# Performance work log

Hardware: AMD Instinct MI355X
Metric: run time of the kernel (lower is better)

The kernel has to match this reference:

```python
import jax, jax.numpy as jnp
import numpy as np

N_NODES = 30000
N_EDGES = 300000
N_GRAPHS = 512
SEQ = 1000
HEADS = 10
CH = 78


def setup_inputs() -> dict:
    key = jax.random.key(0)
    ks = jax.random.split(key, 20)
    def w(k, shape, scale=0.02):
        return jax.random.normal(k, shape, jnp.float32) * scale
    x = jax.random.normal(ks[0], (N_NODES, CH), jnp.float32)
    edge_index = jax.random.randint(ks[1], (2, N_EDGES), 0, N_NODES, jnp.int32)
    # every graph gets a contiguous block of nodes (sorted batch vector)
    batch = (jnp.arange(N_NODES) * N_GRAPHS // N_NODES).astype(jnp.int32)
    target = jax.random.randint(ks[2], (N_GRAPHS, SEQ), 0, 26, jnp.int32)
    return {
        "x": x, "edge_index": edge_index, "batch": batch, "target": target,
        "W_gat": w(ks[3], (CH, HEADS * CH)),
        "att_src": w(ks[4], (HEADS, CH), 0.1),
        "att_dst": w(ks[5], (HEADS, CH), 0.1),
        "b_gat": jnp.zeros((HEADS * CH,), jnp.float32),
        "W_gcn": w(ks[6], (HEADS * CH, HEADS * CH)),
        "b_gcn": jnp.zeros((HEADS * CH,), jnp.float32),
        "W_fcg1": w(ks[7], (2 * HEADS * CH, 1500)), "b_fcg1": jnp.zeros((1500,), jnp.float32),
        "W_fcg2": w(ks[8], (1500, 128)), "b_fcg2": jnp.zeros((128,), jnp.float32),
        "emb": w(ks[9], (26, 128), 1.0),
        "W_conv": w(ks[10], (32, 1000, 8)), "b_conv": jnp.zeros((32,), jnp.float32),
        "W_fcxt": w(ks[11], (32 * 121, 128)), "b_fcxt": jnp.zeros((128,), jnp.float32),
        "W_fc1": w(ks[12], (256, 1024)), "b_fc1": jnp.zeros((1024,), jnp.float32),
        "W_fc2": w(ks[13], (1024, 512)), "b_fc2": jnp.zeros((512,), jnp.float32),
        "W_out": w(ks[14], (512, 1)), "b_out": jnp.zeros((1,), jnp.float32),
    }


def reference(x, edge_index, batch, target,
              W_gat, att_src, att_dst, b_gat, W_gcn, b_gcn,
              W_fcg1, b_fcg1, W_fcg2, b_fcg2, emb, W_conv, b_conv,
              W_fcxt, b_fcxt, W_fc1, b_fc1, W_fc2, b_fc2, W_out, b_out):
    N = x.shape[0]
    loop = jnp.arange(N, dtype=edge_index.dtype)
    src = jnp.concatenate([edge_index[0], loop])  # self-loops (PyG default)
    dst = jnp.concatenate([edge_index[1], loop])

    # ---- GATConv(78 -> 78, heads=10, concat) ----
    h = (x @ W_gat).reshape(N, HEADS, CH)           # [N,H,C]
    a_s = jnp.einsum('nhc,hc->nh', h, att_src)      # [N,H]
    a_d = jnp.einsum('nhc,hc->nh', h, att_dst)
    logits = jax.nn.leaky_relu(a_s[src] + a_d[dst], 0.2)   # [E',H]
    m = jax.ops.segment_max(logits, dst, num_segments=N)
    e = jnp.exp(logits - m[dst])
    denom = jax.ops.segment_sum(e, dst, num_segments=N)
    alpha = e / (denom[dst] + 1e-16)                # per-dst softmax
    xg = jax.ops.segment_sum(h[src] * alpha[:, :, None], dst, num_segments=N)
    xg = jax.nn.relu(xg.reshape(N, HEADS * CH) + b_gat)

    # ---- GCNConv(780 -> 780), symmetric norm with self-loops ----
    deg = jax.ops.segment_sum(jnp.ones_like(dst, dtype=xg.dtype), dst, num_segments=N)
    dinv = jax.lax.rsqrt(jnp.maximum(deg, 1.0))
    norm = dinv[src] * dinv[dst]                    # [E']
    xw = xg @ W_gcn
    xg = jax.ops.segment_sum(xw[src] * norm[:, None], dst, num_segments=N) + b_gcn
    xg = jax.nn.relu(xg)

    # ---- global max + mean pooling per graph ----
    gmax = jax.ops.segment_max(xg, batch, num_segments=N_GRAPHS)
    cnt = jax.ops.segment_sum(jnp.ones((N,), xg.dtype), batch, num_segments=N_GRAPHS)
    gmean = jax.ops.segment_sum(xg, batch, num_segments=N_GRAPHS) / cnt[:, None]
    xp = jnp.concatenate([gmax, gmean], axis=1)     # [G,1560]
    xp = jax.nn.relu(xp @ W_fcg1 + b_fcg1)          # dropout = identity (eval)
    xp = xp @ W_fcg2 + b_fcg2                       # [G,128]

    # ---- protein branch ----
    xt = emb[target]                                # [G,1000,128]
    conv = jax.lax.conv_general_dilated(
        xt, W_conv, window_strides=(1,), padding='VALID',
        dimension_numbers=('NCH', 'OIH', 'NCH'))    # [G,32,121]
    conv = conv + b_conv[None, :, None]
    xt = conv.reshape(conv.shape[0], -1) @ W_fcxt + b_fcxt  # [G,128]

    # ---- joint MLP ----
    xc = jnp.concatenate([xp, xt], axis=1)          # [G,256]
    xc = jax.nn.relu(xc @ W_fc1 + b_fc1)
    xc = jax.nn.relu(xc @ W_fc2 + b_fc2)
    return xc @ W_out + b_out                       # [G,1]
```

## Files before the change

### kernel.cpp

```cpp
#include <hip/hip_runtime.h>
#include <hip/hip_bf16.h>
#include <cstdint>
#include <cstddef>

#define N_NODES 30000
#define E0      300000
#define EPRIME  330000
#define NG      512
#define SEQL    1000
#define HEADS   10
#define CHN     78
#define HC      780
#define HP      800
#define MAXD    64

typedef __attribute__((ext_vector_type(8))) short bf16x8;
typedef __attribute__((ext_vector_type(4))) float f32x4;
typedef __attribute__((ext_vector_type(8))) unsigned short u16x8;

static __device__ __forceinline__ int src_of(const int* ei, int e){
  return (e < E0) ? ei[e] : (e - E0);
}
static __device__ __forceinline__ int dst_of(const int* ei, int e){
  return (e < E0) ? ei[E0 + e] : (e - E0);
}
static __device__ __forceinline__ unsigned short f2bf(float f){
  union { float f; unsigned u; } a; a.f = f;
  unsigned r = a.u + 0x7fff + ((a.u >> 16) & 1);
  return (unsigned short)(r >> 16);
}
static __device__ __forceinline__ float bf2f(unsigned short u){
  union { unsigned u; float f; } a; a.u = ((unsigned)u) << 16; return a.f;
}
static __device__ __forceinline__ void gl_lds16(const unsigned short* g, unsigned short* l){
  __builtin_amdgcn_global_load_lds(
      (const __attribute__((address_space(1))) void*)g,
      (__attribute__((address_space(3))) void*)l,
      16, 0, 0);
}

__global__ void k_bucket(const int* __restrict__ ei, int* __restrict__ cnt, int* __restrict__ bkt){
  int e = blockIdx.x*256 + threadIdx.x;
  if (e < EPRIME){
    int d = dst_of(ei, e);
    int s = src_of(ei, e);
    int slot = atomicAdd(&cnt[d], 1);
    if (slot < MAXD) bkt[d*MAXD + slot] = s;
  }
}

__global__ __launch_bounds__(256) void k_w2t(const float* __restrict__ W_conv, float* __restrict__ w2t){
  int b = blockIdx.x;
  int o = threadIdx.x >> 3, k = threadIdx.x & 7;
  w2t[(size_t)b*256 + threadIdx.x] = W_conv[(size_t)o*8000 + b*8 + k];
}

static __device__ void transp_tile(const float* __restrict__ src, unsigned short* __restrict__ dst,
                                   int K, int N, int Kp, int bx, int by, int hpad){
  __shared__ float t[32][33];
  int k0 = bx*32, n0 = by*32;
  int c = threadIdx.x & 31, r = threadIdx.x >> 5;
  #pragma unroll
  for (int i=0;i<4;i++){
    int k = k0 + r + i*8;
    float v = 0.f;
    if (k < K && n0 + c < N) v = src[(size_t)k*N + n0 + c];
    t[r + i*8][c] = v;
  }
  __syncthreads();
  #pragma unroll
  for (int i=0;i<4;i++){
    int nn = n0 + r + i*8;
    int kk = k0 + c;
    if (nn < N){
      if (hpad){
        if (kk < K){
          int hh = kk/78;
          dst[(size_t)nn*Kp + hh*80 + (kk - hh*78)] = f2bf(t[c][r + i*8]);
        }
      } else {
        if (kk < Kp) dst[(size_t)nn*Kp + kk] = f2bf(t[c][r + i*8]);
      }
    }
  }
}

static __device__ void conv_body(int g, int tid, const int* __restrict__ target,
                                 const float* __restrict__ W2t, const float* __restrict__ emb,
                                 const float* __restrict__ b_conv, float* __restrict__ convf){
  int o = tid >> 3;
  __shared__ int   tgt[SEQL];
  __shared__ int   cntv[26];
  __shared__ int   startv[27];
  __shared__ int   ofs[26];
  __shared__ alignas(16) unsigned short posv[SEQL];
  __shared__ float U[256*26];
  __shared__ float sE[26*128 + 32];

  for (int i = tid; i < 26*128; i += 256) sE[i] = emb[i];
  if (tid < 32) sE[26*128 + tid] = 0.f;
  if (tid < 26) cntv[tid] = 0;
  const int* tg = target + g*SEQL;
  for (int i = tid; i < SEQL; i += 256) tgt[i] = tg[i];
  __syncthreads();
  for (int i = tid; i < SEQL; i += 256) atomicAdd(&cntv[tgt[i]], 1);
  __syncthreads();
  if (tid == 0){
    int s = 0;
    #pragma unroll
    for (int v = 0; v < 26; v++){ startv[v] = s; ofs[v] = s; s += cntv[v]; }
    startv[26] = s;
  }
  __syncthreads();
  for (int i = tid; i < SEQL; i += 256){
    int v = tgt[i];
    int slot = atomicAdd(&ofs[v], 1);
    posv[slot] = (unsigned short)((v << 10) | i);
  }
  __syncthreads();
  {
    const float* wp2 = W2t + tid;
    float s = 0.f;
    int cur = 0;
    for (int j = 0; j < SEQL; j += 8){
      u16x8 p8 = *(const u16x8*)&posv[j];
      float w[8];
      #pragma unroll
      for (int q = 0; q < 8; q++) w[q] = wp2[((int)p8[q] & 1023) << 8];
      #pragma unroll
      for (int q = 0; q < 8; q++){
        int ve = (int)p8[q] >> 10;
        if (ve != cur){
          U[tid*26 + cur] = s;
          for (int z = cur+1; z < ve; z++) U[tid*26 + z] = 0.f;
          cur = ve; s = 0.f;
        }
        s += w[q];
      }
    }
    U[tid*26 + cur] = s;
    for (int z = cur+1; z < 26; z++) U[tid*26 + z] = 0.f;
  }
  __syncthreads();
  int pg = tid & 7;
  int p0 = pg * 16;
  int np = 121 - p0; if (np > 16) np = 16;
  float acc[16];
  #pragma unroll
  for (int i=0;i<16;i++) acc[i]=0.f;
  for (int v = 0; v < 26; v++){
    float u[8];
    #pragma unroll
    for (int kk=0;kk<8;kk++) u[kk] = U[(o*8 + kk)*26 + v];
    const float* ep = &sE[v*128 + p0];
    float e[24];
    #pragma unroll
    for (int i=0;i<24;i+=4){
      float4 q = *(const float4*)(ep + i);
      e[i]=q.x; e[i+1]=q.y; e[i+2]=q.z; e[i+3]=q.w;
    }
    #pragma unroll
    for (int pl=0; pl<16; pl++){
      acc[pl] += u[0]*e[pl]   + u[1]*e[pl+1] + u[2]*e[pl+2] + u[3]*e[pl+3]
               + u[4]*e[pl+4] + u[5]*e[pl+5] + u[6]*e[pl+6] + u[7]*e[pl+7];
    }
  }
  float bo = b_conv[o];
  for (int pl=0; pl<np; pl++)
    convf[(size_t)g*3872 + o*121 + p0 + pl] = acc[pl] + bo;
}

__global__ __launch_bounds__(256) void k_prep(
    const float* __restrict__ x, unsigned short* __restrict__ xb,
    const float* __restrict__ W_gat, unsigned short* __restrict__ wgat_t,
    const float* __restrict__ W_gcn, unsigned short* __restrict__ wgcn_t,
    const float* __restrict__ W_fcg1, unsigned short* __restrict__ wfcg1_t,
    const int* __restrict__ target, const float* __restrict__ w2t,
    const float* __restrict__ emb, const float* __restrict__ b_conv, float* __restrict__ convf,
    unsigned short* __restrict__ xwbp,
    float* __restrict__ xc, float* __restrict__ t1, float* __restrict__ t2, float* __restrict__ fg1,
    const float* __restrict__ b_fcg2, const float* __restrict__ b_fcxt,
    const float* __restrict__ b_fc1, const float* __restrict__ b_fc2,
    const float* __restrict__ b_fcg1, int* __restrict__ cnt)
{
  int b = blockIdx.x;
  int tid = threadIdx.x;
  if (b < 512){ conv_body(b, tid, target, w2t, emb, b_conv, convf); return; }
  b -= 512;
  if (b < 11250){
    int idx = b*256 + tid;
    if (idx < N_NODES*96){
      int n = idx/96, k = idx - n*96;
      xb[idx] = (k < CHN) ? f2bf(x[(size_t)n*CHN + k]) : 0;
    }
    return;
  }
  b -= 11250;
  if (b < 75){ transp_tile(W_gat, wgat_t, CHN, HC, 96, b%3, b/3, 0); return; }
  b -= 75;
  if (b < 625){ transp_tile(W_gcn, wgcn_t, HC, HC, HP, b%25, b/25, 1); return; }
  b -= 625;
  if (b < 2303){ transp_tile(W_fcg1, wfcg1_t, 1560, 1500, 1568, b%49, b/49, 0); return; }
  b -= 2303;
  {
    int g = b;
    int zi = g*256 + tid;
    if (zi < N_NODES) cnt[zi] = 0;
    if (tid < 128){
      xc[(size_t)g*256 + tid]       = b_fcg2[tid];
      xc[(size_t)g*256 + 128 + tid] = b_fcxt[tid];
    }
    for (int i = tid; i < 1024; i += 256) t1[(size_t)g*1024 + i] = b_fc1[i];
    for (int i = tid; i < 512;  i += 256) t2[(size_t)g*512  + i] = b_fc2[i];
    for (int i = tid; i < 1500; i += 256) fg1[(size_t)g*1500 + i] = b_fcg1[i];
    for (int i = tid; i < 59; i += 256){
      int n = g + i*512;
      if (n < N_NODES)
        *reinterpret_cast<unsigned long long*>(xwbp + (size_t)n*HP + HC) = 0ull;
    }
    if (zi < 7800){
      int nn = zi/10, p = zi - (zi/10)*10;
      *reinterpret_cast<unsigned*>(wgcn_t + (size_t)nn*HP + p*80 + 78) = 0u;
    }
  }
}

__global__ __launch_bounds__(256) void k_mfma_bt(
    const unsigned short* __restrict__ A, const unsigned short* __restrict__ Bt,
    const float* __restrict__ bias, float* __restrict__ C, unsigned short* __restrict__ Cb,
    int M, int N, int Kp, int ldc, int relu,
    int ntc, int ntr, int ntk, int Kc, int accum, int hpad)
{
  const int total = ntc*ntr*ntk;
  const int per = (total + 7) >> 3;
  const int b = blockIdx.x;
  const int w = (b & 7)*per + (b >> 3);
  if (w >= total) return;
  const int kt = w / (ntc*ntr);
  const int r2 = w - kt*(ntc*ntr);
  const int row_t = r2 / ntc, col_t = r2 - row_t*ntc;
  const int row0 = row_t*128, col0 = col_t*128;
  const int kbeg = kt*Kc;
  const int kend = min(kbeg + Kc, Kp);

  __shared__ unsigned short As[2][128*32];
  __shared__ unsigned short Bs[2][128*32];
  const int tid = threadIdx.x;
  const int lane = tid & 63;
  const int wv = tid >> 6;
  const int wm = wv >> 1, wn = wv & 1;
  const int quad = lane >> 4, l16 = lane & 15;
  const int srow = lane >> 2;
  const int cidx = lane & 3;
  const int scol = (cidx ^ (srow & 3)) * 8;

  f32x4 acc[4][4];
  #pragma unroll
  for (int mi=0;mi<4;mi++)
    #pragma unroll
    for (int ni=0;ni<4;ni++){
      acc[mi][ni][0]=0.f; acc[mi][ni][1]=0.f; acc[mi][ni][2]=0.f; acc[mi][ni][3]=0.f;
    }

  auto stage = [&](int bsel, int kk){
    #pragma unroll
    for (int i=0;i<2;i++){
      int ch = wv*2 + i;
      int r  = ch*16 + srow;
      gl_lds16(A  + (size_t)(row0 + r)*Kp + kk + scol, &As[bsel][ch*512]);
      gl_lds16(Bt + (size_t)(col0 + r)*Kp + kk + scol, &Bs[bsel][ch*512]);
    }
  };

  const int nt = (kend - kbeg) >> 5;
  stage(0, kbeg);
  __syncthreads();
  int cur = 0;
  for (int t = 0; t < nt; ++t){
    if (t+1 < nt) stage(cur^1, kbeg + ((t+1) << 5));
    bf16x8 af[4], bfr[4];
    #pragma unroll
    for (int mi=0;mi<4;mi++)
      af[mi]  = *(const bf16x8*)(&As[cur][(wm*64 + mi*16 + l16)*32 + ((quad ^ (l16 & 3))*8)]);
    #pragma unroll
    for (int ni=0;ni<4;ni++)
      bfr[ni] = *(const bf16x8*)(&Bs[cur][(wn*64 + ni*16 + l16)*32 + ((quad ^ (l16 & 3))*8)]);
    #pragma unroll
    for (int mi=0;mi<4;mi++)
      #pragma unroll
      for (int ni=0;ni<4;ni++)
        acc[mi][ni] = __builtin_amdgcn_mfma_f32_16x16x32_bf16(af[mi], bfr[ni], acc[mi][ni], 0,0,0);
    __syncthreads();
    cur ^= 1;
  }

  #pragma unroll
  for (int mi=0;mi<4;mi++){
    #pragma unroll
    for (int rr=0;rr<4;rr++){
      int row = row0 + wm*64 + mi*16 + quad*4 + rr;
      if (row >= M) continue;
      #pragma unroll
      for (int ni=0;ni<4;ni++){
        int col = col0 + wn*64 + ni*16 + l16;
        if (col >= N) continue;
        float v = acc[mi][ni][rr];
        if (accum){
          atomicAdd(&C[(size_t)row*ldc + col], v);
        } else {
          if (bias) v += bias[col];
          if (relu) v = fmaxf(v, 0.f);
          int cs = col;
          if (hpad){ int hh = col/78; cs = hh*80 + (col - hh*78); }
          if (Cb) Cb[(size_t)row*ldc + cs] = f2bf(v);
          else    C [(size_t)row*ldc + cs] = v;
        }
      }
    }
  }
}

__global__ __launch_bounds__(256) void k_gemm_sk(const float* __restrict__ A, const float* __restrict__ B,
    float* __restrict__ C, int M, int N, int K, int lda, int ldb, int ldc, int Kc, int relu_a)
{
  __shared__ float As[16][34];
  __shared__ float Bs[16][64];
  const int tid = threadIdx.x;
  const int tx = tid & 15, ty = tid >> 4;
  const int row0 = blockIdx.y * 32, col0 = blockIdx.x * 64;
  const int kbeg = blockIdx.z * Kc;
  const int kend = min(kbeg + Kc, K);
  float acc[2][4];
  #pragma unroll
  for (int i=0;i<2;i++)
    #pragma unroll
    for (int j=0;j<4;j++) acc[i][j] = 0.f;

  for (int k0 = kbeg; k0 < kend; k0 += 16){
    #pragma unroll
    for (int i=0;i<2;i++){
      int idx = tid + i*256;
      int r = idx >> 4, c = idx & 15;
      int gr = row0 + r, gc = k0 + c;
      float v = (gr < M && gc < kend) ? A[(size_t)gr*lda + gc] : 0.f;
      if (relu_a) v = fmaxf(v, 0.f);
      As[c][r] = v;
    }
    #pragma unroll
    for (int i=0;i<4;i++){
      int idx = tid + i*256;
      int r = idx >> 6, c = idx & 63;
      int gr = k0 + r, gc = col0 + c;
      Bs[r][c] = (gr < kend && gc < N) ? B[(size_t)gr*ldb + gc] : 0.f;
    }
    __syncthreads();
    #pragma unroll
    for (int kk=0; kk<16; kk++){
      float a0 = As[kk][ty*2], a1 = As[kk][ty*2+1];
      float b0 = Bs[kk][tx*4], b1 = Bs[kk][tx*4+1], b2 = Bs[kk][tx*4+2], b3 = Bs[kk][tx*4+3];
      acc[0][0]+=a0*b0; acc[0][1]+=a0*b1; acc[0][2]+=a0*b2; acc[0][3]+=a0*b3;
      acc[1][0]+=a1*b0; acc[1][1]+=a1*b1; acc[1][2]+=a1*b2; acc[1][3]+=a1*b3;
    }
    __syncthreads();
  }
  #pragma unroll
  for (int i=0;i<2;i++){
    int r = row0 + ty*2 + i;
    if (r >= M) continue;
    #pragma unroll
    for (int j=0;j<4;j++){
      int c = col0 + tx*4 + j;
      if (c < N) atomicAdd(&C[(size_t)r*ldc + c], acc[i][j]);
    }
  }
}

__global__ __launch_bounds__(256) void k_attn(const unsigned short* __restrict__ hb,
    const float* __restrict__ att_src, const float* __restrict__ att_dst,
    float* __restrict__ a_s, float* __restrict__ a_d){
  __shared__ float ssrc[HC], sdst[HC];
  for (int i = threadIdx.x; i < HC; i += 256){ ssrc[i]=att_src[i]; sdst[i]=att_dst[i]; }
  __syncthreads();
  int idx = blockIdx.x*256 + threadIdx.x;
  if (idx >= N_NODES*HEADS) return;
  int n  = idx / HEADS;
  int hh = idx - n*HEADS;
  const unsigned* hp2 = (const unsigned*)(hb + (size_t)n*HP + hh*80);
  const float* as_ = ssrc + hh*CHN;
  const float* ad_ = sdst + hh*CHN;
  float s1=0.f, s2=0.f;
  #pragma unroll 13
  for (int c2=0;c2<39;c2++){
    unsigned u = hp2[c2];
    float v0 = bf2f((unsigned short)(u & 0xffffu));
    float v1 = bf2f((unsigned short)(u >> 16));
    int c = 2*c2;
    s1 += v0*as_[c] + v1*as_[c+1];
    s2 += v0*ad_[c] + v1*ad_[c+1];
  }
  a_s[idx]=s1; a_d[idx]=s2;
}

__global__ __launch_bounds__(256) void k_gat_agg(
    const unsigned short* __restrict__ hb, const float* __restrict__ a_s, const float* __restrict__ a_d,
    const float* __restrict__ b_gat, const int* __restrict__ cnt, const int* __restrict__ bkt,
    unsigned short* __restrict__ xgb, float* __restrict__ dinv)
{
  int half = threadIdx.x >> 7;
  int lt   = threadIdx.x & 127;
  int n = blockIdx.x*2 + half;
  int deg = cnt[n];
  int degc = min(deg, MAXD);
  __shared__ int   s_src[2][MAXD];
  __shared__ float s_adn[2][HEADS];
  __shared__ float s_lg[2][MAXD*HEADS];
  __shared__ float s_al[2][MAXD*HEADS];
  if (lt < HEADS) s_adn[half][lt] = a_d[(size_t)n*HEADS + lt];
  if (lt < degc)  s_src[half][lt] = bkt[n*MAXD + lt];
  __syncthreads();
  for (int idx = lt; idx < degc*HEADS; idx += 128){
    int j = idx/HEADS, t = idx - j*HEADS;
    float l = a_s[(size_t)s_src[half][j]*HEADS + t] + s_adn[half][t];
    s_lg[half][idx] = (l > 0.f) ? l : 0.2f*l;
  }
  __syncthreads();
  if (lt < HEADS){
    float m = -3.4e38f;
    for (int j=0;j<degc;j++) m = fmaxf(m, s_lg[half][j*HEADS+lt]);
    float s = 0.f;
    for (int j=0;j<degc;j++){ float e = __expf(s_lg[half][j*HEADS+lt]-m); s_al[half][j*HEADS+lt]=e; s+=e; }
    float inv = 1.f/(s + 1e-16f);
    for (int j=0;j<degc;j++) s_al[half][j*HEADS+lt] *= inv;
  }
  __syncthreads();
  if (lt < 100){
    int h = lt/10;
    int r = lt - h*10;
    int nv = (r==9) ? 6 : 8;
    int chb = h*CHN + r*8;
    const float* alp = &s_al[half][h];
    float acc[8];
    #pragma unroll
    for (int e=0;e<8;e++) acc[e]=0.f;
    auto edge = [&](int j){
      int s = s_src[half][j];
      float a = alp[j*HEADS];
      uint4 v = *((const uint4*)(hb + (size_t)s*HP) + lt);
      unsigned uu[4] = {v.x, v.y, v.z, v.w};
      #pragma unroll
      for (int e2=0;e2<4;e2++){
        acc[2*e2]   += a*bf2f((unsigned short)(uu[e2] & 0xffffu));
        acc[2*e2+1] += a*bf2f((unsigned short)(uu[e2] >> 16));
      }
    };
    int j = 0;
    for (; j+2 <= degc; j += 2){ edge(j); edge(j+1); }
    for (; j < degc; ++j) edge(j);
    u16x8 o;
    #pragma unroll
    for (int e=0;e<8;e++){
      float ov = (e < nv) ? fmaxf(acc[e] + b_gat[chb+e], 0.f) : 0.f;
      o[e] = f2bf(ov);
    }
    *((u16x8*)(xgb + (size_t)n*HP) + lt) = o;
  }
  if (lt == 0) dinv[n] = rsqrtf((float)deg);
}

__global__ __launch_bounds__(256) void k_gcn_agg(
    const unsigned short* __restrict__ xwb, const float* __restrict__ dinv, const float* __restrict__ b_gcn,
    const int* __restrict__ cnt, const int* __restrict__ bkt,
    unsigned short* __restrict__ xg2b)
{
  int half = threadIdx.x >> 7;
  int lt   = threadIdx.x & 127;
  int n = blockIdx.x*2 + half;
  int deg = min(cnt[n], MAXD);
  __shared__ int   s_src[2][MAXD];
  __shared__ float s_w[2][MAXD];
  if (lt < deg){
    int s = bkt[n*MAXD + lt];
    s_src[half][lt] = s;
    s_w[half][lt] = dinv[s];
  }
  __syncthreads();
  if (lt < 98){
    int ch0 = lt*8;
    float acc[8];
    #pragma unroll
    for (int e=0;e<8;e++) acc[e]=0.f;
    auto edge = [&](int j){
      int s = s_src[half][j];
      float w = s_w[half][j];
      uint4 v = *((const uint4*)(xwb + (size_t)s*HP) + lt);
      unsigned uu[4] = {v.x, v.y, v.z, v.w};
      #pragma unroll
      for (int e2=0;e2<4;e2++){
        acc[2*e2]   += w*bf2f((unsigned short)(uu[e2] & 0xffffu));
        acc[2*e2+1] += w*bf2f((unsigned short)(uu[e2] >> 16));
      }
    };
    int j = 0;
    for (; j+2 <= deg; j += 2){ edge(j); edge(j+1); }
    for (; j < deg; ++j) edge(j);
    float dn = dinv[n];
    ushort4 o0, o1;
    float r0 = fmaxf(dn*acc[0] + ((ch0   < HC) ? b_gcn[ch0  ] : 0.f), 0.f);
    float r1 = fmaxf(dn*acc[1] + ((ch0+1 < HC) ? b_gcn[ch0+1] : 0.f), 0.f);
    float r2 = fmaxf(dn*acc[2] + ((ch0+2 < HC) ? b_gcn[ch0+2] : 0.f), 0.f);
    float r3 = fmaxf(dn*acc[3] + ((ch0+3 < HC) ? b_gcn[ch0+3] : 0.f), 0.f);
    float r4 = fmaxf(dn*acc[4] + ((ch0+4 < HC) ? b_gcn[ch0+4] : 0.f), 0.f);
    float r5 = fmaxf(dn*acc[5] + ((ch0+5 < HC) ? b_gcn[ch0+5] : 0.f), 0.f);
    float r6 = fmaxf(dn*acc[6] + ((ch0+6 < HC) ? b_gcn[ch0+6] : 0.f), 0.f);
    float r7 = fmaxf(dn*acc[7] + ((ch0+7 < HC) ? b_gcn[ch0+7] : 0.f), 0.f);
    o0.x=f2bf(r0); o0.y=f2bf(r1); o0.z=f2bf(r2); o0.w=f2bf(r3);
    o1.x=f2bf(r4); o1.y=f2bf(r5); o1.z=f2bf(r6); o1.w=f2bf(r7);
    unsigned short* row = xg2b + (size_t)n*HC;
    *(ushort4*)(row + ch0) = o0;
    if (ch0+4 < HC) *(ushort4*)(row + ch0+4) = o1;
  }
}

__global__ __launch_bounds__(256) void k_pool(const unsigned short* __restrict__ xg2b,
                                              unsigned short* __restrict__ xpb){
  int g = blockIdx.x;
  int n0 = (N_NODES*g + NG-1) >> 9;
  int n1 = (N_NODES*(g+1) + NG-1) >> 9;
  float inv = 1.f/(float)(n1 - n0);
  int c4 = threadIdx.x;
  if (c4 < 195){
    const ushort4* x4 = (const ushort4*)xg2b;
    float m0=-3.4e38f,m1=-3.4e38f,m2=-3.4e38f,m3=-3.4e38f;
    float s0=0.f,s1=0.f,s2=0.f,s3=0.f;
    for (int n = n0; n < n1; n++){
      ushort4 v = x4[(size_t)n*195 + c4];
      float a=bf2f(v.x), b=bf2f(v.y), c=bf2f(v.z), d=bf2f(v.w);
      m0=fmaxf(m0,a); m1=fmaxf(m1,b); m2=fmaxf(m2,c); m3=fmaxf(m3,d);
      s0+=a; s1+=b; s2+=c; s3+=d;
    }
    int ch = 4*c4;
    unsigned short* row = xpb + (size_t)g*1568;
    row[ch]=f2bf(m0); row[ch+1]=f2bf(m1); row[ch+2]=f2bf(m2); row[ch+3]=f2bf(m3);
    row[HC+ch]=f2bf(s0*inv); row[HC+ch+1]=f2bf(s1*inv);
    row[HC+ch+2]=f2bf(s2*inv); row[HC+ch+3]=f2bf(s3*inv);
  }
  if (threadIdx.x < 8) xpb[(size_t)g*1568 + 1560 + threadIdx.x] = 0;
}

__global__ __launch_bounds__(64) void k_final(const float* __restrict__ t2, const float* __restrict__ W_out,
                                              const float* __restrict__ b_out, float* __restrict__ out){
  int g = blockIdx.x;
  int lane = threadIdx.x;
  const float* r = t2 + (size_t)g*512;
  float s = 0.f;
  #pragma unroll
  for (int i = lane; i < 512; i += 64) s += fmaxf(r[i], 0.f)*W_out[i];
  #pragma unroll
  for (int off=32; off; off>>=1) s += __shfl_down(s, off);
  if (lane==0) out[g] = s + b_out[0];
}

extern "C" void kernel_launch(void* const* d_in, const int* in_sizes, int n_in,
                              void* d_out, int out_size, void* d_ws, size_t ws_size,
                              hipStream_t stream) {
  const float* x      = (const float*)d_in[0];
  const int*   ei     = (const int*)  d_in[1];
  const int*   target = (const int*)  d_in[3];
  const float* W_gat  = (const float*)d_in[4];
  const float* att_src= (const float*)d_in[5];
  const float* att_dst= (const float*)d_in[6];
  const float* b_gat  = (const float*)d_in[7];
  const float* W_gcn  = (const float*)d_in[8];
  const float* b_gcn  = (const float*)d_in[9];
  const float* W_fcg1 = (const float*)d_in[10];
  const float* b_fcg1 = (const float*)d_in[11];
  const float* W_fcg2 = (const float*)d_in[12];
  const float* b_fcg2 = (const float*)d_in[13];
  const float* emb    = (const float*)d_in[14];
  const float* W_conv = (const float*)d_in[15];
  const float* b_conv = (const float*)d_in[16];
  const float* W_fcxt = (const float*)d_in[17];
  const float* b_fcxt = (const float*)d_in[18];
  const float* W_fc1  = (const float*)d_in[19];
  const float* b_fc1  = (const float*)d_in[20];
  const float* W_fc2  = (const float*)d_in[21];
  const float* b_fc2  = (const float*)d_in[22];
  const float* W_out  = (const float*)d_in[23];
  const float* b_out  = (const float*)d_in[24];
  float* out = (float*)d_out;

  char* ws = (char*)d_ws;
  size_t off = 0;
  auto alloc = [&](size_t bytes)->char*{
    char* p = ws + off;
    off += (bytes + 255) & ~(size_t)255;
    return p;
  };
  unsigned short* hb  = (unsigned short*)alloc((size_t)N_NODES*HP*2);
  unsigned short* xwb = (unsigned short*)alloc((size_t)N_NODES*HP*2);
  unsigned short* xu  = (unsigned short*)alloc((size_t)N_NODES*HP*2);
  unsigned short* xb     = (unsigned short*)alloc((size_t)N_NODES*96*2);
  unsigned short* wgat_t = (unsigned short*)alloc((size_t)HC*96*2);
  unsigned short* wgcn_t = (unsigned short*)alloc((size_t)HC*HP*2);
  unsigned short* wfcg1_t= (unsigned short*)alloc((size_t)1500*1568*2);
  unsigned short* xpb    = (unsigned short*)alloc((size_t)NG*1568*2);
  float* a_s    = (float*)alloc((size_t)N_NODES*HEADS*4);
  float* a_d    = (float*)alloc((size_t)N_NODES*HEADS*4);
  float* dinv   = (float*)alloc((size_t)N_NODES*4);
  int*   cnt    = (int*)  alloc((size_t)N_NODES*4);
  int*   bkt    = (int*)  alloc((size_t)N_NODES*MAXD*4);
  float* fg1    = (float*)alloc((size_t)NG*1500*4);
  float* convf  = (float*)alloc((size_t)NG*3872*4);
  float* xc     = (float*)alloc((size_t)NG*256*4);
  float* t1     = (float*)alloc((size_t)NG*1024*4);
  float* t2     = (float*)alloc((size_t)NG*512*4);
  float* w2t    = (float*)alloc((size_t)SEQL*256*4);

  unsigned short* xgb  = xu;
  unsigned short* xg2b = xu;

  k_w2t<<<1000, 256, 0, stream>>>(W_conv, w2t);

  k_prep<<<512+11250+75+625+2303+512, 256, 0, stream>>>(
      x, xb, W_gat, wgat_t, W_gcn, wgcn_t, W_fcg1, wfcg1_t,
      target, w2t, emb, b_conv, convf, xwb,
      xc, t1, t2, fg1, b_fcg2, b_fcxt, b_fc1, b_fc2, b_fcg1, cnt);

  k_bucket<<<(EPRIME+255)/256, 256, 0, stream>>>(ei, cnt, bkt);

  auto swgrid = [](int total){ return 8 * ((total + 7) / 8); };

  k_mfma_bt<<<swgrid(7*235), 256, 0, stream>>>(xb, wgat_t, nullptr, nullptr, hb,
                                               N_NODES, HC, 96, HP, 0, 7, 235, 1, 96, 0, 1);
  k_attn<<<(N_NODES*HEADS+255)/256, 256, 0, stream>>>(hb, att_src, att_dst, a_s, a_d);
  k_gat_agg<<<N_NODES/2, 256, 0, stream>>>(hb, a_s, a_d, b_gat, cnt, bkt, xgb, dinv);

  k_mfma_bt<<<swgrid(7*235), 256, 0, stream>>>(xgb, wgcn_t, nullptr, nullptr, xwb,
                                               N_NODES, HC, HP, HP, 0, 7, 235, 1, HP, 0, 0);
  k_gcn_agg<<<N_NODES/2, 256, 0, stream>>>(xwb, dinv, b_gcn, cnt, bkt, xg2b);

  k_pool<<<NG, 256, 0, stream>>>(xg2b, xpb);
  k_mfma_bt<<<swgrid(12*4*2), 256, 0, stream>>>(xpb, wfcg1_t, nullptr, fg1, nullptr,
                                                NG, 1500, 1568, 1500, 0, 12, 4, 2, 800, 1, 0);
  k_gemm_sk<<<dim3(2, 16, 8), 256, 0, stream>>>(fg1, W_fcg2, xc, NG, 128, 1500, 1500, 128, 256, 192, 1);

  k_gemm_sk<<<dim3(2, 16, 8), 256, 0, stream>>>(convf, W_fcxt, xc + 128, NG, 128, 3872, 3872, 128, 256, 512, 0);

  k_gemm_sk<<<dim3(16, 16, 1), 256, 0, stream>>>(xc, W_fc1, t1, NG, 1024, 256, 256, 1024, 1024, 256, 0);
  k_gemm_sk<<<dim3(8, 16, 2), 256, 0, stream>>>(t1, W_fc2, t2, NG, 512, 1024, 1024, 512, 512, 512, 1);
  k_final<<<NG, 64, 0, stream>>>(t2, W_out, b_out, out);
}
```

Before: 814.4 us.

## Compute conv weight sums in registers and batch gather loads in aggregations

The conv body no longer builds a 256x26 shared U table in a separate pass. Each thread now sums its 8 conv weights per vocabulary bucket directly from global memory using float4 loads, which saves shared memory and a barrier. In exchange, every thread group of 8 re-reads weights per output channel instead of sharing them. The GAT and GCN aggregation loops now issue four row gathers before doing the multiply-adds, so more memory loads are in flight at once, at the cost of extra registers.

```diff
diff --git a/kernel.cpp b/kernel.cpp
--- a/kernel.cpp
+++ b/kernel.cpp
@@ -94,7 +94,6 @@
   __shared__ int   startv[27];
   __shared__ int   ofs[26];
   __shared__ alignas(16) unsigned short posv[SEQL];
-  __shared__ float U[256*26];
   __shared__ float sE[26*128 + 32];
 
   for (int i = tid; i < 26*128; i += 256) sE[i] = emb[i];
@@ -115,54 +114,39 @@
   for (int i = tid; i < SEQL; i += 256){
     int v = tgt[i];
     int slot = atomicAdd(&ofs[v], 1);
-    posv[slot] = (unsigned short)((v << 10) | i);
-  }
-  __syncthreads();
-  {
-    const float* wp2 = W2t + tid;
-    float s = 0.f;
-    int cur = 0;
-    for (int j = 0; j < SEQL; j += 8){
-      u16x8 p8 = *(const u16x8*)&posv[j];
-      float w[8];
-      #pragma unroll
-      for (int q = 0; q < 8; q++) w[q] = wp2[((int)p8[q] & 1023) << 8];
-      #pragma unroll
-      for (int q = 0; q < 8; q++){
-        int ve = (int)p8[q] >> 10;
-        if (ve != cur){
-          U[tid*26 + cur] = s;
-          for (int z = cur+1; z < ve; z++) U[tid*26 + z] = 0.f;
-          cur = ve; s = 0.f;
-        }
-        s += w[q];
-      }
-    }
-    U[tid*26 + cur] = s;
-    for (int z = cur+1; z < 26; z++) U[tid*26 + z] = 0.f;
-  }
-  __syncthreads();
+    posv[slot] = (unsigned short)i;
+  }
+  __syncthreads();
+
   int pg = tid & 7;
   int p0 = pg * 16;
   int np = 121 - p0; if (np > 16) np = 16;
+  const float* wp8 = W2t + o*8;
   float acc[16];
   #pragma unroll
   for (int i=0;i<16;i++) acc[i]=0.f;
+  int j = 0;
   for (int v = 0; v < 26; v++){
-    float u[8];
-    #pragma unroll
-    for (int kk=0;kk<8;kk++) u[kk] = U[(o*8 + kk)*26 + v];
+    int e_end = startv[v+1];
+    float s0=0.f,s1=0.f,s2=0.f,s3=0.f,s4=0.f,s5=0.f,s6=0.f,s7=0.f;
+    for (; j < e_end; ++j){
+      const float* wp = wp8 + ((int)posv[j] << 8);
+      float4 wa = *(const float4*)wp;
+      float4 wb = *(const float4*)(wp+4);
+      s0+=wa.x; s1+=wa.y; s2+=wa.z; s3+=wa.w;
+      s4+=wb.x; s5+=wb.y; s6+=wb.z; s7+=wb.w;
+    }
     const float* ep = &sE[v*128 + p0];
     float e[24];
     #pragma unroll
-    for (int i=0;i<24;i+=4){
-      float4 q = *(const float4*)(ep + i);
-      e[i]=q.x; e[i+1]=q.y; e[i+2]=q.z; e[i+3]=q.w;
+    for (int i2=0;i2<24;i2+=4){
+      float4 q = *(const float4*)(ep + i2);
+      e[i2]=q.x; e[i2+1]=q.y; e[i2+2]=q.z; e[i2+3]=q.w;
     }
     #pragma unroll
     for (int pl=0; pl<16; pl++){
-      acc[pl] += u[0]*e[pl]   + u[1]*e[pl+1] + u[2]*e[pl+2] + u[3]*e[pl+3]
-               + u[4]*e[pl+4] + u[5]*e[pl+5] + u[6]*e[pl+6] + u[7]*e[pl+7];
+      acc[pl] += s0*e[pl]   + s1*e[pl+1] + s2*e[pl+2] + s3*e[pl+3]
+               + s4*e[pl+4] + s5*e[pl+5] + s6*e[pl+6] + s7*e[pl+7];
     }
   }
   float bo = b_conv[o];
@@ -442,10 +426,12 @@
     float acc[8];
     #pragma unroll
     for (int e=0;e<8;e++) acc[e]=0.f;
-    auto edge = [&](int j){
+    auto ld = [&](int j, uint4& v, float& a){
       int s = s_src[half][j];
-      float a = alp[j*HEADS];
-      uint4 v = *((const uint4*)(hb + (size_t)s*HP) + lt);
+      a = alp[j*HEADS];
+      v = *((const uint4*)(hb + (size_t)s*HP) + lt);
+    };
+    auto fm = [&](const uint4& v, float a){
       unsigned uu[4] = {v.x, v.y, v.z, v.w};
       #pragma unroll
       for (int e2=0;e2<4;e2++){
@@ -454,8 +440,21 @@
       }
     };
     int j = 0;
-    for (; j+2 <= degc; j += 2){ edge(j); edge(j+1); }
-    for (; j < degc; ++j) edge(j);
+    for (; j+4 <= degc; j += 4){
+      uint4 v0,v1,v2,v3; float a0,a1,a2,a3;
+      ld(j,v0,a0); ld(j+1,v1,a1); ld(j+2,v2,a2); ld(j+3,v3,a3);
+      fm(v0,a0); fm(v1,a1); fm(v2,a2); fm(v3,a3);
+    }
+    if (j+2 <= degc){
+      uint4 v0,v1; float a0,a1;
+      ld(j,v0,a0); ld(j+1,v1,a1);
+      fm(v0,a0); fm(v1,a1);
+      j += 2;
+    }
+    if (j < degc){
+      uint4 v0; float a0;
+      ld(j,v0,a0); fm(v0,a0);
+    }
     u16x8 o;
     #pragma unroll
     for (int e=0;e<8;e++){
@@ -489,20 +488,35 @@
     float acc[8];
     #pragma unroll
     for (int e=0;e<8;e++) acc[e]=0.f;
-    auto edge = [&](int j){
+    auto ld = [&](int j, uint4& v, float& a){
       int s = s_src[half][j];
-      float w = s_w[half][j];
-      uint4 v = *((const uint4*)(xwb + (size_t)s*HP) + lt);
+      a = s_w[half][j];
+      v = *((const uint4*)(xwb + (size_t)s*HP) + lt);
+    };
+    auto fm = [&](const uint4& v, float a){
       unsigned uu[4] = {v.x, v.y, v.z, v.w};
       #pragma unroll
       for (int e2=0;e2<4;e2++){
-        acc[2*e2]   += w*bf2f((unsigned short)(uu[e2] & 0xffffu));
-        acc[2*e2+1] += w*bf2f((unsigned short)(uu[e2] >> 16));
+        acc[2*e2]   += a*bf2f((unsigned short)(uu[e2] & 0xffffu));
+        acc[2*e2+1] += a*bf2f((unsigned short)(uu[e2] >> 16));
       }
     };
     int j = 0;
-    for (; j+2 <= deg; j += 2){ edge(j); edge(j+1); }
-    for (; j < deg; ++j) edge(j);
+    for (; j+4 <= deg; j += 4){
+      uint4 v0,v1,v2,v3; float a0,a1,a2,a3;
+      ld(j,v0,a0); ld(j+1,v1,a1); ld(j+2,v2,a2); ld(j+3,v3,a3);
+      fm(v0,a0); fm(v1,a1); fm(v2,a2); fm(v3,a3);
+    }
+    if (j+2 <= deg){
+      uint4 v0,v1; float a0,a1;
+      ld(j,v0,a0); ld(j+1,v1,a1);
+      fm(v0,a0); fm(v1,a1);
+      j += 2;
+    }
+    if (j < deg){
+      uint4 v0; float a0;
+      ld(j,v0,a0); fm(v0,a0);
+    }
     float dn = dinv[n];
     ushort4 o0, o1;
     float r0 = fmaxf(dn*acc[0] + ((ch0   < HC) ? b_gcn[ch0  ] : 0.f), 0.f);
```

Result: slower. 907.6 us (+11.4%).
